# Performance work log

Measured on AMD Instinct MI355X. Metric: run time of the kernel, lower is better.

The kernel has to match this reference:

```python
import jax, jax.numpy as jnp
import numpy as np

# ---- static configuration (matches init_kwargs) ----
B = 32
H = 56
W = 56
C = 192
HEADS = 6
WS = 7            # window size
SHIFT = 3         # shift size (WS // 2)
MLP_HIDDEN = 768  # 4 * C
CPB = 256         # clip(56*56//16, 256, 1024)
N = WS * WS       # tokens per window
NW = (H // WS) * (W // WS)  # windows per image
EPS = 1e-5

# ---- static tables (Swin V2 continuous relative position bias) ----
# log-spaced relative coords table: [(2*WS-1)^2, 2]
_r = np.arange(-(WS - 1), WS, dtype=np.float32)
_tab = np.stack(np.meshgrid(_r, _r, indexing='ij'), axis=-1)  # [2WS-1, 2WS-1, 2]
_tab = _tab / (WS - 1) * 8.0  # pretrained_window_size=0 -> use window_size-1
_tab = np.sign(_tab) * np.log2(np.abs(_tab) + 1.0) / np.log2(8.0)
REL_TABLE = jnp.asarray(_tab.reshape(-1, 2))

# relative position index: [N, N] into the (2WS-1)^2 table
_coords = np.stack(np.meshgrid(np.arange(WS), np.arange(WS), indexing='ij'))
_cf = _coords.reshape(2, -1)
_rel = (_cf[:, :, None] - _cf[:, None, :]).transpose(1, 2, 0).astype(np.int64)
_rel[..., 0] += WS - 1
_rel[..., 1] += WS - 1
_rel[..., 0] *= 2 * WS - 1
REL_INDEX = jnp.asarray(_rel.sum(-1))

# shifted-window attention mask: [NW, N, N] with 0 / -100
_img = np.zeros((H, W), dtype=np.float32)
_sl = [slice(0, -WS), slice(-WS, -SHIFT), slice(-SHIFT, None)]
_cnt = 0
for _hs in _sl:
    for _ws in _sl:
        _img[_hs, _ws] = _cnt
        _cnt += 1
_mw = _img.reshape(H // WS, WS, W // WS, WS).transpose(0, 2, 1, 3).reshape(-1, N)
_am = _mw[:, None, :] - _mw[:, :, None]
ATTN_MASK = jnp.asarray(np.where(_am != 0, -100.0, 0.0).astype(np.float32))


def _layer_norm(x, g, b):
    mu = jnp.mean(x, axis=-1, keepdims=True)
    var = jnp.mean(jnp.square(x - mu), axis=-1, keepdims=True)
    return (x - mu) * jax.lax.rsqrt(var + EPS) * g + b


def setup_inputs() -> dict:
    key = jax.random.key(0)
    ks = jax.random.split(key, 10)
    def n(k, shape, s=0.02):
        return jax.random.normal(k, shape, jnp.float32) * s
    return {
        'x': jax.random.normal(ks[0], (B, H * W, C), jnp.float32),
        'qkv_w': n(ks[1], (3 * C, C)),
        'q_bias': jnp.zeros((C,), jnp.float32),
        'v_bias': jnp.zeros((C,), jnp.float32),
        'logit_scale': jnp.full((HEADS, 1, 1), jnp.log(10.0), jnp.float32),
        'cpb_w1': n(ks[2], (CPB, 2)),
        'cpb_b1': jnp.zeros((CPB,), jnp.float32),
        'cpb_w2': n(ks[3], (HEADS, CPB)),
        'proj_w': n(ks[4], (C, C)),
        'proj_b': jnp.zeros((C,), jnp.float32),
        'norm1_g': jnp.ones((C,), jnp.float32),
        'norm1_b': jnp.zeros((C,), jnp.float32),
        'norm2_g': jnp.ones((C,), jnp.float32),
        'norm2_b': jnp.zeros((C,), jnp.float32),
        'fc1_w': n(ks[5], (MLP_HIDDEN, C)),
        'fc1_b': jnp.zeros((MLP_HIDDEN,), jnp.float32),
        'fc2_w': n(ks[6], (C, MLP_HIDDEN)),
        'fc2_b': jnp.zeros((C,), jnp.float32),
    }


def reference(x, qkv_w, q_bias, v_bias, logit_scale, cpb_w1, cpb_b1, cpb_w2,
              proj_w, proj_b, norm1_g, norm1_b, norm2_g, norm2_b,
              fc1_w, fc1_b, fc2_w, fc2_b):
    b = x.shape[0]
    hd = C // HEADS
    shortcut = x

    # cyclic shift + window partition -> [b*NW, N, C]
    xi = jnp.roll(x.reshape(b, H, W, C), (-SHIFT, -SHIFT), axis=(1, 2))
    xw = xi.reshape(b, H // WS, WS, W // WS, WS, C)
    xw = xw.transpose(0, 1, 3, 2, 4, 5).reshape(-1, N, C)

    # qkv projection (k has no bias, per Swin V2)
    qkv_bias = jnp.concatenate([q_bias, jnp.zeros_like(q_bias), v_bias])
    qkv = (xw @ qkv_w.T + qkv_bias).reshape(-1, N, 3, HEADS, hd)
    qkv = qkv.transpose(2, 0, 3, 1, 4)  # [3, bw, heads, N, hd]
    q, k, v = qkv[0], qkv[1], qkv[2]

    # cosine attention with learned logit scale
    q = q / jnp.maximum(jnp.linalg.norm(q, axis=-1, keepdims=True), 1e-12)
    k = k / jnp.maximum(jnp.linalg.norm(k, axis=-1, keepdims=True), 1e-12)
    scale = jnp.exp(jnp.minimum(logit_scale, jnp.log(100.0)))  # [heads,1,1]
    attn = jnp.einsum('bhnd,bhmd->bhnm', q, k) * scale

    # continuous relative position bias via tiny MLP
    tab = jax.nn.relu(REL_TABLE @ cpb_w1.T + cpb_b1) @ cpb_w2.T  # [(2WS-1)^2, heads]
    rpb = 16.0 * jax.nn.sigmoid(tab[REL_INDEX])                  # [N, N, heads]
    attn = attn + rpb.transpose(2, 0, 1)[None]

    # shifted-window mask + softmax
    attn = attn.reshape(-1, NW, HEADS, N, N) + ATTN_MASK[None, :, None]
    attn = jax.nn.softmax(attn.reshape(-1, HEADS, N, N), axis=-1)

    out = jnp.einsum('bhnm,bhmd->bhnd', attn, v)
    out = out.transpose(0, 2, 1, 3).reshape(-1, N, C) @ proj_w.T + proj_b

    # window reverse + reverse shift
    xr = out.reshape(b, H // WS, W // WS, WS, WS, C)
    xr = xr.transpose(0, 1, 3, 2, 4, 5).reshape(b, H, W, C)
    xr = jnp.roll(xr, (SHIFT, SHIFT), axis=(1, 2)).reshape(b, H * W, C)

    # post-norm residual (Swin V2 style)
    x1 = shortcut + _layer_norm(xr, norm1_g, norm1_b)
    hmid = jax.nn.silu(x1 @ fc1_w.T + fc1_b) @ fc2_w.T + fc2_b
    return x1 + _layer_norm(hmid, norm2_g, norm2_b)
```

## Files before the change

kernel.cpp:

```cpp
#include <hip/hip_runtime.h>


typedef unsigned short ushort_t;
using f32x4  = __attribute__((ext_vector_type(4))) float;
using short8 = __attribute__((ext_vector_type(8))) short;

#define GLOAD(srcp, ldsp) __builtin_amdgcn_global_load_lds(                    \
    (const __attribute__((address_space(1))) void*)(srcp),                     \
    (__attribute__((address_space(3))) void*)(ldsp), 16, 0, 0)

__device__ __forceinline__ ushort_t f2bf(float f) {
  union { float f; unsigned u; } v; v.f = f;
  unsigned r = v.u + 0x7fffu + ((v.u >> 16) & 1u);
  return (ushort_t)(r >> 16);
}
__device__ __forceinline__ float bf2f(ushort_t u) {
  union { unsigned u; float f; } v; v.u = ((unsigned)u) << 16;
  return v.f;
}
__device__ __forceinline__ int slot32(int k) {
  return 8 * ((k & 15) >> 2) + ((k >> 4) << 2) + (k & 3);
}

__device__ __forceinline__ int img_pos(int m) {
  int win = m / 49, n = m - win * 49;
  int b = win >> 6, wi = win & 63;
  int nd = n / 7, nm = n - nd * 7;
  int hs = (wi >> 3) * 7 + nd;
  int ws = (wi & 7) * 7 + nm;
  int h = hs + 3; if (h >= 56) h -= 56;
  int w = ws + 3; if (w >= 56) w -= 56;
  return b * 3136 + h * 56 + w;
}

__device__ __forceinline__ int region3(int a) { return a < 49 ? 0 : (a < 53 ? 1 : 2); }

__global__ void cvt_perm_kernel(const float* __restrict__ in, ushort_t* __restrict__ out,
                                int n, int K) {
  int i = blockIdx.x * 256 + threadIdx.x;
  if (i >= n) return;
  int row = i / K, j = i - row * K;
  int s = (j & ~31) + slot32(j & 31);
  out[row * K + s] = f2bf(in[i]);
}

__global__ __launch_bounds__(256) void gather_cvt_kernel(
    const float* __restrict__ x, ushort_t* __restrict__ xw) {
  int i8 = blockIdx.x * 256 + threadIdx.x;
  int m = i8 / 24, c8 = (i8 - m * 24) * 8;
  const float* p = x + (size_t)img_pos(m) * 192 + c8;
  float4 a = *(const float4*)p, b = *(const float4*)(p + 4);
  ushort_t* q = xw + (size_t)m * 192;
  int blk = c8 & ~31;
  int jj = (c8 & 31) >> 3;
  int b4 = ((jj & 1) << 4) | ((jj >> 1) << 2);
  *(ushort4*)(q + blk + b4)     = make_ushort4(f2bf(a.x), f2bf(a.y), f2bf(a.z), f2bf(a.w));
  *(ushort4*)(q + blk + b4 + 8) = make_ushort4(f2bf(b.x), f2bf(b.y), f2bf(b.z), f2bf(b.w));
}

__global__ __launch_bounds__(256) void cpb_kernel(
    const float* __restrict__ w1, const float* __restrict__ b1,
    const float* __restrict__ w2, float* __restrict__ tab_s) {
  int e = blockIdx.x;
  int t = threadIdx.x;
  int i = e / 13, j = e - 13 * (e / 13);
  auto cval = [](int a) -> float {
    float r = (a - 6) * (8.0f / 6.0f);
    float v = log2f(fabsf(r) + 1.f) * (1.f / 3.f);
    return r < 0.f ? -v : v;
  };
  float ci = cval(i), cj = cval(j);
  float h = fmaxf(ci * w1[2 * t] + cj * w1[2 * t + 1] + b1[t], 0.f);
  __shared__ float red[256];
  for (int head = 0; head < 6; ++head) {
    red[t] = h * w2[head * 256 + t];
    __syncthreads();
    for (int st = 128; st > 0; st >>= 1) {
      if (t < st) red[t] += red[t + st];
      __syncthreads();
    }
    if (t == 0) tab_s[head * 169 + e] = 16.f / (1.f + __expf(-red[0]));
    __syncthreads();
  }
}

template<int KTOT, int MODE>
__global__ __launch_bounds__(512, 4) void gemm_g512(
    const ushort_t* __restrict__ Ab, const ushort_t* __restrict__ W,
    const float* __restrict__ b0, const float* __restrict__ b1,
    ushort_t* out, int NTOT) {
  __shared__ ushort_t Al[2][4096];
  __shared__ ushort_t Bl[2][6144];
  int t = threadIdx.x;
  int m0 = blockIdx.x * 128, n0 = blockIdx.y * 192;
  int lane = t & 63, wid = t >> 6;
  int wm = wid >> 1, wn = wid & 1;
  int lr = lane & 15, lg = lane >> 4;

  bool stager = (t < 256);
  int sw = (t & 255) >> 6;
  int rloc = lane >> 2;
  int csrc = (lane & 3) ^ ((lane >> 3) & 3);
  int ca = sw * 2, cb = sw * 3;
  const ushort_t* sA0 = Ab + (size_t)(m0 + ca * 16      + rloc) * KTOT + csrc * 8;
  const ushort_t* sA1 = Ab + (size_t)(m0 + ca * 16 + 16 + rloc) * KTOT + csrc * 8;
  const ushort_t* sB0 = W  + (size_t)(n0 + cb * 16      + rloc) * KTOT + csrc * 8;
  const ushort_t* sB1 = W  + (size_t)(n0 + cb * 16 + 16 + rloc) * KTOT + csrc * 8;
  const ushort_t* sB2 = W  + (size_t)(n0 + cb * 16 + 32 + rloc) * KTOT + csrc * 8;

  auto STAGE = [&](int buf, int kt) {
    GLOAD(sA0 + kt, &Al[buf][(ca + 0) * 512]);
    GLOAD(sA1 + kt, &Al[buf][(ca + 1) * 512]);
    GLOAD(sB0 + kt, &Bl[buf][(cb + 0) * 512]);
    GLOAD(sB1 + kt, &Bl[buf][(cb + 1) * 512]);
    GLOAD(sB2 + kt, &Bl[buf][(cb + 2) * 512]);
  };

  int coff = (lg ^ ((lr >> 1) & 3)) * 8;

  f32x4 acc[2][6];
#pragma unroll
  for (int a = 0; a < 2; ++a)
#pragma unroll
    for (int b = 0; b < 6; ++b) acc[a][b] = (f32x4){0.f, 0.f, 0.f, 0.f};

  const int NT = KTOT / 32;
  if (stager) STAGE(0, 0);
  __syncthreads();
  int cur = 0;
  for (int it = 0; it < NT; ++it) {
    if (stager && it + 1 < NT) STAGE(cur ^ 1, (it + 1) * 32);
    short8 af[2], bfv[6];
#pragma unroll
    for (int fm = 0; fm < 2; ++fm)
      af[fm] = *(const short8*)&Al[cur][(wm * 32 + fm * 16 + lr) * 32 + coff];
#pragma unroll
    for (int fn = 0; fn < 6; ++fn)
      bfv[fn] = *(const short8*)&Bl[cur][(wn * 96 + fn * 16 + lr) * 32 + coff];
#pragma unroll
    for (int fm = 0; fm < 2; ++fm)
#pragma unroll
      for (int fn = 0; fn < 6; ++fn)
        acc[fm][fn] = __builtin_amdgcn_mfma_f32_16x16x32_bf16(af[fm], bfv[fn], acc[fm][fn], 0, 0, 0);
    __syncthreads();
    cur ^= 1;
  }

#pragma unroll
  for (int fm = 0; fm < 2; ++fm) {
#pragma unroll
    for (int fn = 0; fn < 6; ++fn) {
      int col = n0 + wn * 96 + fn * 16 + lr;
      int colp = n0 + wn * 96 + ((fn >> 1) << 5) +
                 ((lr >> 2) << 3) + ((fn & 1) << 2) + (lr & 3);
      float bias;
      if (MODE == 0) bias = (col < 192) ? b0[col] : ((col < 384) ? 0.f : b1[col - 384]);
      else           bias = b0[col];
#pragma unroll
      for (int r = 0; r < 4; ++r) {
        int row = m0 + wm * 32 + fm * 16 + lg * 4 + r;
        float v = acc[fm][fn][r] + bias;
        if (MODE == 1) v = v / (1.f + __expf(-v));
        out[(size_t)row * NTOT + colp] = f2bf(v);
      }
    }
  }
}

__global__ __launch_bounds__(512, 4) void gemm_g512_lnfc2(
    const ushort_t* __restrict__ Ab, const ushort_t* __restrict__ W,
    const float* __restrict__ bias, const float* __restrict__ gamma,
    const float* __restrict__ beta, const ushort_t* __restrict__ residb,
    float* __restrict__ outf) {
  const int KTOT = 768;
  __shared__ ushort_t Al[2][4096];
  __shared__ ushort_t Bl[2][6144];
  int t = threadIdx.x;
  int m0 = blockIdx.x * 128;
  int lane = t & 63, wid = t >> 6;
  int wm = wid >> 1, wn = wid & 1;
  int lr = lane & 15, lg = lane >> 4;

  bool stager = (t < 256);
  int sw = (t & 255) >> 6;
  int rloc = lane >> 2;
  int csrc = (lane & 3) ^ ((lane >> 3) & 3);
  int ca = sw * 2, cb = sw * 3;
  const ushort_t* sA0 = Ab + (size_t)(m0 + ca * 16      + rloc) * KTOT + csrc * 8;
  const ushort_t* sA1 = Ab + (size_t)(m0 + ca * 16 + 16 + rloc) * KTOT + csrc * 8;
  const ushort_t* sB0 = W  + (size_t)(cb * 16      + rloc) * KTOT + csrc * 8;
  const ushort_t* sB1 = W  + (size_t)(cb * 16 + 16 + rloc) * KTOT + csrc * 8;
  const ushort_t* sB2 = W  + (size_t)(cb * 16 + 32 + rloc) * KTOT + csrc * 8;

  auto STAGE = [&](int buf, int kt) {
    GLOAD(sA0 + kt, &Al[buf][(ca + 0) * 512]);
    GLOAD(sA1 + kt, &Al[buf][(ca + 1) * 512]);
    GLOAD(sB0 + kt, &Bl[buf][(cb + 0) * 512]);
    GLOAD(sB1 + kt, &Bl[buf][(cb + 1) * 512]);
    GLOAD(sB2 + kt, &Bl[buf][(cb + 2) * 512]);
  };

  int coff = (lg ^ ((lr >> 1) & 3)) * 8;

  f32x4 acc[2][6];
#pragma unroll
  for (int a = 0; a < 2; ++a)
#pragma unroll
    for (int b = 0; b < 6; ++b) acc[a][b] = (f32x4){0.f, 0.f, 0.f, 0.f};

  const int NT = KTOT / 32;
  if (stager) STAGE(0, 0);
  __syncthreads();
  int cur = 0;
  for (int it = 0; it < NT; ++it) {
    if (stager && it + 1 < NT) STAGE(cur ^ 1, (it + 1) * 32);
    short8 af[2], bfv[6];
#pragma unroll
    for (int fm = 0; fm < 2; ++fm)
      af[fm] = *(const short8*)&Al[cur][(wm * 32 + fm * 16 + lr) * 32 + coff];
#pragma unroll
    for (int fn = 0; fn < 6; ++fn)
      bfv[fn] = *(const short8*)&Bl[cur][(wn * 96 + fn * 16 + lr) * 32 + coff];
#pragma unroll
    for (int fm = 0; fm < 2; ++fm)
#pragma unroll
      for (int fn = 0; fn < 6; ++fn)
        acc[fm][fn] = __builtin_amdgcn_mfma_f32_16x16x32_bf16(af[fm], bfv[fn], acc[fm][fn], 0, 0, 0);
    __syncthreads();
    cur ^= 1;
  }

  float* part = (float*)&Bl[0][0];
#pragma unroll
  for (int fm = 0; fm < 2; ++fm) {
#pragma unroll
    for (int r = 0; r < 4; ++r) {
      float s1 = 0.f, s2 = 0.f;
#pragma unroll
      for (int fn = 0; fn < 6; ++fn) {
        int col = wn * 96 + fn * 16 + lr;
        float v = acc[fm][fn][r] + bias[col];
        acc[fm][fn][r] = v;
        s1 += v; s2 += v * v;
      }
#pragma unroll
      for (int off = 1; off < 16; off <<= 1) {
        s1 += __shfl_xor(s1, off);
        s2 += __shfl_xor(s2, off);
      }
      if (lr == 0) {
        int lrow = wm * 32 + fm * 16 + lg * 4 + r;
        part[(wn * 128 + lrow) * 2 + 0] = s1;
        part[(wn * 128 + lrow) * 2 + 1] = s2;
      }
    }
  }
  __syncthreads();
#pragma unroll
  for (int fm = 0; fm < 2; ++fm) {
#pragma unroll
    for (int r = 0; r < 4; ++r) {
      int lrow = wm * 32 + fm * 16 + lg * 4 + r;
      float s1 = part[lrow * 2 + 0] + part[(128 + lrow) * 2 + 0];
      float s2 = part[lrow * 2 + 1] + part[(128 + lrow) * 2 + 1];
      float mean = s1 * (1.f / 192.f);
      float var  = s2 * (1.f / 192.f) - mean * mean;
      float rstd = rsqrtf(fmaxf(var, 0.f) + 1e-5f);
      size_t og = (size_t)(m0 + lrow) * 192;
#pragma unroll
      for (int fn = 0; fn < 6; ++fn) {
        int col = wn * 96 + fn * 16 + lr;
        int colp = (col & ~31) + slot32(col & 31);
        float l = (acc[fm][fn][r] - mean) * rstd * gamma[col] + beta[col];
        outf[og + col] = bf2f(residb[og + colp]) + l;
      }
    }
  }
}

__global__ __launch_bounds__(256) void ln_resid_kernel(
    const ushort_t* __restrict__ pre, const float* __restrict__ residf,
    const float* __restrict__ gamma, const float* __restrict__ beta,
    ushort_t* __restrict__ outb) {
  int m = (blockIdx.x * 256 + threadIdx.x) >> 6;
  int lane = threadIdx.x & 63;
  int c0 = lane, c1 = lane + 64, c2 = lane + 128;
  int s0 = (c0 & ~31) + slot32(c0 & 31);
  int s1c = (c1 & ~31) + slot32(c1 & 31);
  int s2c = (c2 & ~31) + slot32(c2 & 31);
  const ushort_t* p = pre + (size_t)m * 192;
  float v0 = bf2f(p[s0]), v1 = bf2f(p[s1c]), v2 = bf2f(p[s2c]);
  float s1 = v0 + v1 + v2;
  float s2 = v0 * v0 + v1 * v1 + v2 * v2;
#pragma unroll
  for (int o = 1; o < 64; o <<= 1) {
    s1 += __shfl_xor(s1, o);
    s2 += __shfl_xor(s2, o);
  }
  float mean = s1 * (1.f / 192.f);
  float var  = s2 * (1.f / 192.f) - mean * mean;
  float rstd = rsqrtf(fmaxf(var, 0.f) + 1e-5f);
  float l0 = (v0 - mean) * rstd * gamma[c0] + beta[c0];
  float l1 = (v1 - mean) * rstd * gamma[c1] + beta[c1];
  float l2 = (v2 - mean) * rstd * gamma[c2] + beta[c2];
  size_t og = (size_t)img_pos(m) * 192;
  outb[og + s0]  = f2bf(residf[og + c0] + l0);
  outb[og + s1c] = f2bf(residf[og + c1] + l1);
  outb[og + s2c] = f2bf(residf[og + c2] + l2);
}

__global__ __launch_bounds__(256) void attn_kernel(
    const ushort_t* __restrict__ qkv, const float* __restrict__ logit_scale,
    const float* __restrict__ tab_s, ushort_t* __restrict__ attn_out) {
  __shared__ ushort_t qs[64][40];
  __shared__ ushort_t ksl[64][40];
  __shared__ ushort_t vsl[32][80];
  __shared__ ushort_t ps[64][80];
  __shared__ float tab_l[169];
  int win = blockIdx.x, head = blockIdx.y;
  int t = threadIdx.x;
  int wi = win & 63;
  int wh0 = (wi >> 3) * 7, ww0 = (wi & 7) * 7;
  size_t base = (size_t)win * 49 * 576 + head * 32;

  for (int u = t; u < 169; u += 256) tab_l[u] = tab_s[head * 169 + u];

  for (int u = t; u < 240; u += 256) {
    int arr = u / 120, v = u - arr * 120;
    int r = 49 + (v >> 3), c4 = (v & 7) << 2;
    ushort_t* p = arr ? &ksl[r][c4] : &qs[r][c4];
    *(ushort4*)p = make_ushort4(0, 0, 0, 0);
  }

  for (int u = t; u < 2048; u += 256) {
    int key = u >> 5, d = u & 31;
    ushort_t val = 0;
    if (key < 49) val = qkv[base + (size_t)key * 576 + 384 + d];
    int kk = key & 31;
    int pc = ((key >> 5) << 5) + 8 * ((kk >> 2) & 3) + 4 * (kk >> 4) + (kk & 3);
    vsl[d][pc] = val;
  }

  float scale = __expf(fminf(logit_scale[head], 4.605170186f));

  if (t < 196) {
    int r = t >> 2, c = t & 3;
    const ushort_t* qp = qkv + base + (size_t)r * 576 + c * 8;
    ushort4 qa = *(const ushort4*)qp,         qb = *(const ushort4*)(qp + 4);
    ushort4 ka = *(const ushort4*)(qp + 192), kb = *(const ushort4*)(qp + 196);
    float qf[8] = {bf2f(qa.x), bf2f(qa.y), bf2f(qa.z), bf2f(qa.w),
                   bf2f(qb.x), bf2f(qb.y), bf2f(qb.z), bf2f(qb.w)};
    float kf[8] = {bf2f(ka.x), bf2f(ka.y), bf2f(ka.z), bf2f(ka.w),
                   bf2f(kb.x), bf2f(kb.y), bf2f(kb.z), bf2f(kb.w)};
    float sq = 0.f, sk = 0.f;
#pragma unroll
    for (int d = 0; d < 8; ++d) { sq += qf[d] * qf[d]; sk += kf[d] * kf[d]; }
    sq += __shfl_xor(sq, 1); sq += __shfl_xor(sq, 2);
    sk += __shfl_xor(sk, 1); sk += __shfl_xor(sk, 2);
    float rq = scale / fmaxf(sqrtf(sq), 1e-12f);
    float rk = 1.f   / fmaxf(sqrtf(sk), 1e-12f);
    ushort_t* qd = &qs[r][c * 8];
    *(ushort4*)(qd + 0) = make_ushort4(f2bf(qf[0]*rq), f2bf(qf[1]*rq), f2bf(qf[2]*rq), f2bf(qf[3]*rq));
    *(ushort4*)(qd + 4) = make_ushort4(f2bf(qf[4]*rq), f2bf(qf[5]*rq), f2bf(qf[6]*rq), f2bf(qf[7]*rq));
    ushort_t* kd = &ksl[r][c * 8];
    *(ushort4*)(kd + 0) = make_ushort4(f2bf(kf[0]*rk), f2bf(kf[1]*rk), f2bf(kf[2]*rk), f2bf(kf[3]*rk));
    *(ushort4*)(kd + 4) = make_ushort4(f2bf(kf[4]*rk), f2bf(kf[5]*rk), f2bf(kf[6]*rk), f2bf(kf[7]*rk));
  }
  __syncthreads();

  int lane = t & 63, w = t >> 6;
  int lr = lane & 15, lg = lane >> 4;

  short8 aq = *(const short8*)&qs[w * 16 + lr][lg * 8];
  f32x4 acc[4];
#pragma unroll
  for (int fn = 0; fn < 4; ++fn) {
    acc[fn] = (f32x4){0.f, 0.f, 0.f, 0.f};
    short8 bk = *(const short8*)&ksl[fn * 16 + lr][lg * 8];
    acc[fn] = __builtin_amdgcn_mfma_f32_16x16x32_bf16(aq, bk, acc[fn], 0, 0, 0);
  }

  float rsum[4];
#pragma unroll
  for (int r = 0; r < 4; ++r) {
    int row = w * 16 + lg * 4 + r;
    int rd = (row * 9363) >> 16, rm = row - 7 * rd;
    int gr = region3(wh0 + rd) * 3 + region3(ww0 + rm);
    bool rv = row < 49;
    float sv[4];
#pragma unroll
    for (int fn = 0; fn < 4; ++fn) {
      int col = fn * 16 + lr;
      int jd = (col * 9363) >> 16, jm = col - 7 * jd;
      int gj = region3(wh0 + jd) * 3 + region3(ww0 + jm);
      bool cv = rv && (col < 49);
      int idx = cv ? (rd - jd + 6) * 13 + (rm - jm + 6) : 0;
      float s = acc[fn][r] + tab_l[idx] + (gr == gj ? 0.f : -100.f);
      sv[fn] = cv ? s : -1e30f;
    }
    float m = fmaxf(fmaxf(sv[0], sv[1]), fmaxf(sv[2], sv[3]));
#pragma unroll
    for (int o = 1; o < 16; o <<= 1) m = fmaxf(m, __shfl_xor(m, o));
    float sum = 0.f;
#pragma unroll
    for (int fn = 0; fn < 4; ++fn) {
      float e = __expf(sv[fn] - m);
      sum += e;
      int pc = ((fn >> 1) << 5) + 8 * (lr >> 2) + ((fn & 1) << 2) + (lr & 3);
      ps[row][pc] = f2bf(e);
    }
#pragma unroll
    for (int o = 1; o < 16; o <<= 1) sum += __shfl_xor(sum, o);
    rsum[r] = 1.f / sum;
  }
  __syncthreads();

  short8 ap0 = *(const short8*)&ps[w * 16 + lr][lg * 8];
  short8 ap1 = *(const short8*)&ps[w * 16 + lr][32 + lg * 8];
  f32x4 o2[2];
#pragma unroll
  for (int f = 0; f < 2; ++f) {
    o2[f] = (f32x4){0.f, 0.f, 0.f, 0.f};
    short8 bv0 = *(const short8*)&vsl[f * 16 + lr][lg * 8];
    short8 bv1 = *(const short8*)&vsl[f * 16 + lr][32 + lg * 8];
    o2[f] = __builtin_amdgcn_mfma_f32_16x16x32_bf16(ap0, bv0, o2[f], 0, 0, 0);
    o2[f] = __builtin_amdgcn_mfma_f32_16x16x32_bf16(ap1, bv1, o2[f], 0, 0, 0);
  }
#pragma unroll
  for (int f = 0; f < 2; ++f) {
#pragma unroll
    for (int r = 0; r < 4; ++r) {
      int row = w * 16 + lg * 4 + r;
      if (row < 49)
        attn_out[((size_t)win * 49 + row) * 192 + head * 32 + f * 16 + lr] =
            f2bf(o2[f][r] * rsum[r]);
    }
  }
}

extern "C" void kernel_launch(void* const* d_in, const int* in_sizes, int n_in,
                              void* d_out, int out_size, void* d_ws, size_t ws_size,
                              hipStream_t stream) {
  (void)in_sizes; (void)n_in; (void)out_size; (void)ws_size;
  const float* x    = (const float*)d_in[0];
  const float* qkvw = (const float*)d_in[1];
  const float* qb   = (const float*)d_in[2];
  const float* vb   = (const float*)d_in[3];
  const float* ls   = (const float*)d_in[4];
  const float* cw1  = (const float*)d_in[5];
  const float* cb1  = (const float*)d_in[6];
  const float* cw2  = (const float*)d_in[7];
  const float* pw   = (const float*)d_in[8];
  const float* pb   = (const float*)d_in[9];
  const float* n1g  = (const float*)d_in[10];
  const float* n1b  = (const float*)d_in[11];
  const float* n2g  = (const float*)d_in[12];
  const float* n2b  = (const float*)d_in[13];
  const float* f1w  = (const float*)d_in[14];
  const float* f1b  = (const float*)d_in[15];
  const float* f2w  = (const float*)d_in[16];
  const float* f2b  = (const float*)d_in[17];
  float* out = (float*)d_out;

  char* ws = (char*)d_ws;
  ushort_t* wq_bf = (ushort_t*)ws;
  ushort_t* wp_bf = wq_bf + 110592;
  ushort_t* w1_bf = wp_bf + 36864;
  ushort_t* w2_bf = w1_bf + 147456;
  float*    tab_s = (float*)(w2_bf + 147456);
  const size_t OFF_BIG = 1 << 20;
  ushort_t* qkv_out = (ushort_t*)(ws + OFF_BIG);
  ushort_t* xw_bf   = (ushort_t*)(ws + OFF_BIG + 115605504);
  ushort_t* attn_o  = (ushort_t*)(ws + OFF_BIG + 115605504);
  ushort_t* x1_bf   = (ushort_t*)(ws + OFF_BIG + 154140672);
  ushort_t* hmid    = (ushort_t*)(ws + OFF_BIG);

  cvt_perm_kernel<<<(110592 + 255) / 256, 256, 0, stream>>>(qkvw, wq_bf, 110592, 192);
  cvt_perm_kernel<<<(36864  + 255) / 256, 256, 0, stream>>>(pw,   wp_bf, 36864, 192);
  cvt_perm_kernel<<<(147456 + 255) / 256, 256, 0, stream>>>(f1w,  w1_bf, 147456, 192);
  cvt_perm_kernel<<<(147456 + 255) / 256, 256, 0, stream>>>(f2w,  w2_bf, 147456, 768);
  cpb_kernel<<<169, 256, 0, stream>>>(cw1, cb1, cw2, tab_s);
  gather_cvt_kernel<<<9408, 256, 0, stream>>>(x, xw_bf);

  gemm_g512<192, 0><<<dim3(784, 3), 512, 0, stream>>>(xw_bf, wq_bf, qb, vb, qkv_out, 576);
  attn_kernel<<<dim3(2048, 6), 256, 0, stream>>>(qkv_out, ls, tab_s, attn_o);
  gemm_g512<192, 2><<<dim3(784, 1), 512, 0, stream>>>(attn_o, wp_bf, pb, nullptr, attn_o, 192);
  ln_resid_kernel<<<25088, 256, 0, stream>>>(attn_o, x, n1g, n1b, x1_bf);
  gemm_g512<192, 1><<<dim3(784, 4), 512, 0, stream>>>(x1_bf, w1_bf, f1b, nullptr, hmid, 768);
  gemm_g512_lnfc2<<<784, 512, 0, stream>>>(hmid, w2_bf, f2b, n2g, n2b, x1_bf, out);
}
```

Before: 363.3 us.

## Add triple-buffered GEMM for QKV and FC1, merge weight conversion kernels

```diff
diff --git a/kernel.cpp b/kernel.cpp
--- a/kernel.cpp
+++ b/kernel.cpp
@@ -35,13 +35,20 @@
 
 __device__ __forceinline__ int region3(int a) { return a < 49 ? 0 : (a < 53 ? 1 : 2); }
 
-__global__ void cvt_perm_kernel(const float* __restrict__ in, ushort_t* __restrict__ out,
-                                int n, int K) {
+__global__ __launch_bounds__(256) void cvt_perm_all(
+    const float* __restrict__ qkvw, const float* __restrict__ pw,
+    const float* __restrict__ f1w, const float* __restrict__ f2w,
+    ushort_t* __restrict__ wq, ushort_t* __restrict__ wp,
+    ushort_t* __restrict__ w1, ushort_t* __restrict__ w2) {
   int i = blockIdx.x * 256 + threadIdx.x;
-  if (i >= n) return;
-  int row = i / K, j = i - row * K;
-  int s = (j & ~31) + slot32(j & 31);
-  out[row * K + s] = f2bf(in[i]);
+  if (i >= 442368) return;
+  const float* in; ushort_t* out; int K, j;
+  if (i < 110592)      { j = i;          in = qkvw; out = wq; K = 192; }
+  else if (i < 147456) { j = i - 110592; in = pw;   out = wp; K = 192; }
+  else if (i < 294912) { j = i - 147456; in = f1w;  out = w1; K = 192; }
+  else                 { j = i - 294912; in = f2w;  out = w2; K = 768; }
+  int row = j / K, c = j - row * K;
+  out[row * K + (c & ~31) + slot32(c & 31)] = f2bf(in[j]);
 }
 
 __global__ __launch_bounds__(256) void gather_cvt_kernel(
@@ -81,6 +88,101 @@
     }
     if (t == 0) tab_s[head * 169 + e] = 16.f / (1.f + __expf(-red[0]));
     __syncthreads();
+  }
+}
+
+template<int KTOT, int MODE>
+__global__ __launch_bounds__(512, 4) void gemm_p3(
+    const ushort_t* __restrict__ Ab, const ushort_t* __restrict__ W,
+    const float* __restrict__ b0, const float* __restrict__ b1,
+    ushort_t* __restrict__ out, int NTOT) {
+  __shared__ ushort_t Al[3][4096];
+  __shared__ ushort_t Bl[3][6144];
+  int t = threadIdx.x;
+  int m0 = blockIdx.x * 128, n0 = blockIdx.y * 192;
+  int lane = t & 63, wid = t >> 6;
+  int wm = wid >> 1, wn = wid & 1;
+  int lr = lane & 15, lg = lane >> 4;
+
+  bool stager = (t < 256);
+  int sw = (t & 255) >> 6;
+  int rloc = lane >> 2;
+  int csrc = (lane & 3) ^ ((lane >> 3) & 3);
+  int ca = sw * 2, cb = sw * 3;
+  const ushort_t* sA0 = Ab + (size_t)(m0 + ca * 16      + rloc) * KTOT + csrc * 8;
+  const ushort_t* sA1 = Ab + (size_t)(m0 + ca * 16 + 16 + rloc) * KTOT + csrc * 8;
+  const ushort_t* sB0 = W  + (size_t)(n0 + cb * 16      + rloc) * KTOT + csrc * 8;
+  const ushort_t* sB1 = W  + (size_t)(n0 + cb * 16 + 16 + rloc) * KTOT + csrc * 8;
+  const ushort_t* sB2 = W  + (size_t)(n0 + cb * 16 + 32 + rloc) * KTOT + csrc * 8;
+
+  auto STAGE = [&](int buf, int kt) {
+    GLOAD(sA0 + kt, &Al[buf][(ca + 0) * 512]);
+    GLOAD(sA1 + kt, &Al[buf][(ca + 1) * 512]);
+    GLOAD(sB0 + kt, &Bl[buf][(cb + 0) * 512]);
+    GLOAD(sB1 + kt, &Bl[buf][(cb + 1) * 512]);
+    GLOAD(sB2 + kt, &Bl[buf][(cb + 2) * 512]);
+  };
+
+  int coff = (lg ^ ((lr >> 1) & 3)) * 8;
+
+  f32x4 acc[2][6];
+#pragma unroll
+  for (int a = 0; a < 2; ++a)
+#pragma unroll
+    for (int b = 0; b < 6; ++b) acc[a][b] = (f32x4){0.f, 0.f, 0.f, 0.f};
+
+  const int NT = KTOT / 32;
+  if (stager) { STAGE(0, 0); STAGE(1, 32); }
+  for (int it = 0; it < NT; ++it) {
+    int cur = it % 3;
+    if (stager) {
+      if (it + 2 < NT) {
+        STAGE((it + 2) % 3, (it + 2) * 32);
+        asm volatile("s_waitcnt vmcnt(10)" ::: "memory");
+      } else if (it + 1 < NT) {
+        asm volatile("s_waitcnt vmcnt(5)" ::: "memory");
+      } else {
+        asm volatile("s_waitcnt vmcnt(0)" ::: "memory");
+      }
+    }
+    __builtin_amdgcn_sched_barrier(0);
+    __builtin_amdgcn_s_barrier();
+    __builtin_amdgcn_sched_barrier(0);
+    short8 af[2], bfv[6];
+#pragma unroll
+    for (int fm = 0; fm < 2; ++fm)
+      af[fm] = *(const short8*)&Al[cur][(wm * 32 + fm * 16 + lr) * 32 + coff];
+#pragma unroll
+    for (int fn = 0; fn < 6; ++fn)
+      bfv[fn] = *(const short8*)&Bl[cur][(wn * 96 + fn * 16 + lr) * 32 + coff];
+#pragma unroll
+    for (int fm = 0; fm < 2; ++fm)
+#pragma unroll
+      for (int fn = 0; fn < 6; ++fn)
+        acc[fm][fn] = __builtin_amdgcn_mfma_f32_16x16x32_bf16(af[fm], bfv[fn], acc[fm][fn], 0, 0, 0);
+    __builtin_amdgcn_sched_barrier(0);
+    __builtin_amdgcn_s_barrier();
+    __builtin_amdgcn_sched_barrier(0);
+  }
+
+#pragma unroll
+  for (int fm = 0; fm < 2; ++fm) {
+#pragma unroll
+    for (int fn = 0; fn < 6; ++fn) {
+      int col = n0 + wn * 96 + fn * 16 + lr;
+      int colp = n0 + wn * 96 + ((fn >> 1) << 5) +
+                 ((lr >> 2) << 3) + ((fn & 1) << 2) + (lr & 3);
+      float bias;
+      if (MODE == 0) bias = (col < 192) ? b0[col] : ((col < 384) ? 0.f : b1[col - 384]);
+      else           bias = b0[col];
+#pragma unroll
+      for (int r = 0; r < 4; ++r) {
+        int row = m0 + wm * 32 + fm * 16 + lg * 4 + r;
+        float v = acc[fm][fn][r] + bias;
+        if (MODE == 1) v = v / (1.f + __expf(-v));
+        out[(size_t)row * NTOT + colp] = f2bf(v);
+      }
+    }
   }
 }
 
@@ -475,17 +577,14 @@
   ushort_t* x1_bf   = (ushort_t*)(ws + OFF_BIG + 154140672);
   ushort_t* hmid    = (ushort_t*)(ws + OFF_BIG);
 
-  cvt_perm_kernel<<<(110592 + 255) / 256, 256, 0, stream>>>(qkvw, wq_bf, 110592, 192);
-  cvt_perm_kernel<<<(36864  + 255) / 256, 256, 0, stream>>>(pw,   wp_bf, 36864, 192);
-  cvt_perm_kernel<<<(147456 + 255) / 256, 256, 0, stream>>>(f1w,  w1_bf, 147456, 192);
-  cvt_perm_kernel<<<(147456 + 255) / 256, 256, 0, stream>>>(f2w,  w2_bf, 147456, 768);
+  cvt_perm_all<<<1728, 256, 0, stream>>>(qkvw, pw, f1w, f2w, wq_bf, wp_bf, w1_bf, w2_bf);
   cpb_kernel<<<169, 256, 0, stream>>>(cw1, cb1, cw2, tab_s);
   gather_cvt_kernel<<<9408, 256, 0, stream>>>(x, xw_bf);
 
-  gemm_g512<192, 0><<<dim3(784, 3), 512, 0, stream>>>(xw_bf, wq_bf, qb, vb, qkv_out, 576);
+  gemm_p3<192, 0><<<dim3(784, 3), 512, 0, stream>>>(xw_bf, wq_bf, qb, vb, qkv_out, 576);
   attn_kernel<<<dim3(2048, 6), 256, 0, stream>>>(qkv_out, ls, tab_s, attn_o);
   gemm_g512<192, 2><<<dim3(784, 1), 512, 0, stream>>>(attn_o, wp_bf, pb, nullptr, attn_o, 192);
   ln_resid_kernel<<<25088, 256, 0, stream>>>(attn_o, x, n1g, n1b, x1_bf);
-  gemm_g512<192, 1><<<dim3(784, 4), 512, 0, stream>>>(x1_bf, w1_bf, f1b, nullptr, hmid, 768);
+  gemm_p3<192, 1><<<dim3(784, 4), 512, 0, stream>>>(x1_bf, w1_bf, f1b, nullptr, hmid, 768);
   gemm_g512_lnfc2<<<784, 512, 0, stream>>>(hmid, w2_bf, f2b, n2g, n2b, x1_bf, out);
 }
```

Result: no change. 359.1 us (-1.2%).
